# Optimization experiments

Measured on AMD Instinct MI355X. Metric: run time of the kernel, lower is better.

The kernel has to match this reference:

```python
import jax, jax.numpy as jnp
from jax import lax
import numpy as np

B, V, T, K, HE, TH, E, L = 128, 30000, 50, 50, 256, 800, 300, 3
DELTA = 0.005


def setup_inputs() -> dict:
    key = jax.random.key(0)
    ks = jax.random.split(key, 24)
    rn = lambda k, s, sc=0.05: jax.random.normal(k, s, jnp.float32) * sc
    return dict(
        X=jax.random.uniform(ks[0], (B, V), jnp.float32),
        timestamp=jax.random.randint(ks[1], (B,), 0, T),
        X_mean=jax.random.uniform(ks[2], (T, V), jnp.float32),
        W_eta_map=rn(ks[3], (HE, V)), b_eta_map=rn(ks[4], (HE,)),
        lstm_Wih=rn(ks[5], (L, 4 * HE, HE)), lstm_Whh=rn(ks[6], (L, 4 * HE, HE)),
        lstm_bih=rn(ks[7], (L, 4 * HE)), lstm_bhh=rn(ks[8], (L, 4 * HE)),
        W_qeta_mu=rn(ks[9], (K, HE + K)), b_qeta_mu=rn(ks[10], (K,)),
        W_qeta_ls=rn(ks[11], (K, HE + K)), b_qeta_ls=rn(ks[12], (K,)),
        W1=rn(ks[13], (TH, V + K)), b1=rn(ks[14], (TH,)),
        W2=rn(ks[15], (TH, TH)), b2=rn(ks[16], (TH,)),
        W_qt_mu=rn(ks[17], (K, TH)), b_qt_mu=rn(ks[18], (K,)),
        W_qt_ls=rn(ks[19], (K, TH)), b_qt_ls=rn(ks[20], (K,)),
        mu_q_alpha=rn(ks[21], (K, T, E), 0.1),
        logsigma_q_alpha=rn(ks[22], (K, T, E), 0.1),
        emb=rn(ks[23], (V, E), 0.1),
    )


def _lstm(x, Wih, Whh, bih, bhh):
    # PyTorch-style multi-layer LSTM, batch=1 squeezed away; x: [T, HE]
    for l in range(Wih.shape[0]):
        Wi, Wh, bi, bh = Wih[l], Whh[l], bih[l], bhh[l]
        def step(carry, xt, Wi=Wi, Wh=Wh, bi=bi, bh=bh):
            h, c = carry
            g = Wi @ xt + Wh @ h + bi + bh
            i, f, gg, o = jnp.split(g, 4)  # torch gate order i,f,g,o
            c = jax.nn.sigmoid(f) * c + jax.nn.sigmoid(i) * jnp.tanh(gg)
            h = jax.nn.sigmoid(o) * jnp.tanh(c)
            return (h, c), h
        H = Wh.shape[1]
        _, x = lax.scan(step, (jnp.zeros(H, x.dtype), jnp.zeros(H, x.dtype)), x)
    return x


def reference(X, timestamp, X_mean, W_eta_map, b_eta_map, lstm_Wih, lstm_Whh,
              lstm_bih, lstm_bhh, W_qeta_mu, b_qeta_mu, W_qeta_ls, b_qeta_ls,
              W1, b1, W2, b2, W_qt_mu, b_qt_mu, W_qt_ls, b_qt_ls,
              mu_q_alpha, logsigma_q_alpha, emb):
    # eval-mode DETM forward (reparameterize returns mu when not training)
    nb = X / X.sum(1, keepdims=True)
    logd = jnp.log(jnp.float32(DELTA))
    Tn = X_mean.shape[0]
    first = jnp.arange(Tn) == 0

    # --- eta: LSTM over time then sequential Gaussian recurrence ---
    rnn_out = _lstm(X_mean @ W_eta_map.T + b_eta_map, lstm_Wih, lstm_Whh, lstm_bih, lstm_bhh)  # [T,HE]
    Kn = W_qeta_mu.shape[0]

    def eta_step(eta_prev, xs):
        out_t, f = xs
        h = jnp.concatenate([out_t, eta_prev])
        mu = W_qeta_mu @ h + b_qeta_mu
        ls = W_qeta_ls @ h + b_qeta_ls
        p_ls = jnp.where(f, 0.0, logd)  # prior: N(0,I) at t=0, N(eta_{t-1}, delta) after
        kl = 0.5 * jnp.sum((jnp.exp(ls) + (mu - eta_prev) ** 2) / (jnp.exp(p_ls) + 1e-6) - 1.0 + p_ls - ls)
        return mu, (mu, kl)  # eval: eta_t = mu_t

    _, (etas, kls_eta) = lax.scan(eta_step, jnp.zeros(Kn, X.dtype), (rnn_out, first))
    kl_eta = kls_eta.sum()

    # --- theta ---
    eta_td = etas[timestamp]  # [B,K]
    h = jnp.tanh(jnp.concatenate([nb, eta_td], axis=1) @ W1.T + b1)
    h = jnp.tanh(h @ W2.T + b2)
    mu_t = h @ W_qt_mu.T + b_qt_mu
    ls_t = h @ W_qt_ls.T + b_qt_ls
    theta = jax.nn.softmax(mu_t, axis=-1)  # eval: z = mu
    kl_theta = (0.5 * jnp.sum((jnp.exp(ls_t) + (mu_t - eta_td) ** 2) / (1.0 + 1e-6) - 1.0 - ls_t, axis=-1)).sum()

    # --- alpha (eval: alpha_t = mu_q_alpha[:,t,:]) ---
    alphas = jnp.transpose(mu_q_alpha, (1, 0, 2))      # [T,K,E]
    q_ls = jnp.transpose(logsigma_q_alpha, (1, 0, 2))
    p_mu = jnp.concatenate([jnp.zeros_like(alphas[:1]), alphas[:-1]], axis=0)
    p_ls = jnp.where(first[:, None, None], 0.0, logd)
    kl_alpha = (0.5 * jnp.sum((jnp.exp(q_ls) + (alphas - p_mu) ** 2) / (jnp.exp(p_ls) + 1e-6) - 1.0 + p_ls - q_ls, axis=-1)).sum()

    # --- beta, likelihood ---
    beta = jax.nn.softmax(jnp.einsum('tke,ve->tkv', alphas, emb), axis=-1)  # [T,K,V]
    px = jnp.einsum('bk,bkv->bv', theta, beta[timestamp])
    lnpx = jnp.log(px + 1e-6)
    nll = (-lnpx * X).sum(-1).mean()
    return theta, lnpx, beta, nll, kl_alpha, kl_eta, kl_theta
```

## Files before the change

kernel.cpp:

```cpp
#include <hip/hip_runtime.h>
#include <math.h>

#define B_  128
#define V_  30000
#define T_  50
#define K_  50
#define HE_ 256
#define TH_ 800
#define E_  300
#define L_  3

#define LOGD_ (-5.2983173665480363f)

#define TM 64
#define TN 64
#define TK 16

__global__ __launch_bounds__(256) void gemm_nt(
    const float* __restrict__ A, int lda, int M,
    const float* __restrict__ B, int ldb, int N,
    int K,
    float* __restrict__ C, int ldc,
    const float* __restrict__ bias, int mode, int kchunk)
{
    __shared__ float As[TK][TM + 4];
    __shared__ float Bs[TK][TN + 4];
    const int tid = threadIdx.x;
    const int bm = blockIdx.y * TM;
    const int bn = blockIdx.x * TN;
    const int tx = tid & 15;
    const int ty = tid >> 4;
    const int lr = tid >> 2;
    const int lc = (tid & 3) << 2;

    float acc[4][4];
#pragma unroll
    for (int i = 0; i < 4; ++i)
#pragma unroll
        for (int j = 0; j < 4; ++j) acc[i][j] = 0.f;

    const int kbeg = blockIdx.z * kchunk;
    const int kend = min(K, kbeg + kchunk);

    for (int k0 = kbeg; k0 < kend; k0 += TK) {
        {
            float v0 = 0.f, v1 = 0.f, v2 = 0.f, v3 = 0.f;
            int gr = bm + lr;
            if (gr < M) {
                const float* p = A + (size_t)gr * lda + k0 + lc;
                int rem = K - (k0 + lc);
                if (rem >= 4) {
                    float2 a0 = *(const float2*)p;
                    float2 a1 = *(const float2*)(p + 2);
                    v0 = a0.x; v1 = a0.y; v2 = a1.x; v3 = a1.y;
                } else {
                    if (rem > 0) v0 = p[0];
                    if (rem > 1) v1 = p[1];
                    if (rem > 2) v2 = p[2];
                }
            }
            As[lc + 0][lr] = v0; As[lc + 1][lr] = v1;
            As[lc + 2][lr] = v2; As[lc + 3][lr] = v3;
        }
        {
            float v0 = 0.f, v1 = 0.f, v2 = 0.f, v3 = 0.f;
            int gr = bn + lr;
            if (gr < N) {
                const float* p = B + (size_t)gr * ldb + k0 + lc;
                int rem = K - (k0 + lc);
                if (rem >= 4) {
                    float2 a0 = *(const float2*)p;
                    float2 a1 = *(const float2*)(p + 2);
                    v0 = a0.x; v1 = a0.y; v2 = a1.x; v3 = a1.y;
                } else {
                    if (rem > 0) v0 = p[0];
                    if (rem > 1) v1 = p[1];
                    if (rem > 2) v2 = p[2];
                }
            }
            Bs[lc + 0][lr] = v0; Bs[lc + 1][lr] = v1;
            Bs[lc + 2][lr] = v2; Bs[lc + 3][lr] = v3;
        }
        __syncthreads();
#pragma unroll
        for (int kk = 0; kk < TK; ++kk) {
            float a[4], b[4];
#pragma unroll
            for (int i = 0; i < 4; ++i) a[i] = As[kk][ty * 4 + i];
#pragma unroll
            for (int j = 0; j < 4; ++j) b[j] = Bs[kk][tx * 4 + j];
#pragma unroll
            for (int i = 0; i < 4; ++i)
#pragma unroll
                for (int j = 0; j < 4; ++j) acc[i][j] += a[i] * b[j];
        }
        __syncthreads();
    }

#pragma unroll
    for (int i = 0; i < 4; ++i) {
        int row = bm + ty * 4 + i;
        if (row >= M) continue;
#pragma unroll
        for (int j = 0; j < 4; ++j) {
            int col = bn + tx * 4 + j;
            if (col >= N) continue;
            float v = acc[i][j];
            if (mode == 3) {
                atomicAdd(&C[(size_t)row * ldc + col], v);
            } else {
                if (mode == 1) v = tanhf(v + bias[col]);
                else if (mode == 2) v = v + bias[col];
                C[(size_t)row * ldc + col] = v;
            }
        }
    }
}

__global__ __launch_bounds__(256) void bias_act(
    float* __restrict__ C, const float* __restrict__ bias,
    int total, int N, int mode)
{
    int idx = blockIdx.x * 256 + threadIdx.x;
    if (idx >= total) return;
    int j = idx % N;
    float v = C[idx] + bias[j];
    if (mode == 1) v = tanhf(v);
    C[idx] = v;
}

__global__ __launch_bounds__(256) void rowsum_inv(const float* __restrict__ X,
                                                  float* __restrict__ inv)
{
    int b = blockIdx.x;
    const float4* p = (const float4*)(X + (size_t)b * V_);
    float s = 0.f;
    for (int i = threadIdx.x; i < V_ / 4; i += 256) {
        float4 v = p[i];
        s += v.x + v.y + v.z + v.w;
    }
    for (int off = 32; off; off >>= 1) s += __shfl_down(s, off);
    __shared__ float red[4];
    int wid = threadIdx.x >> 6, lane = threadIdx.x & 63;
    if (lane == 0) red[wid] = s;
    __syncthreads();
    if (threadIdx.x == 0) inv[b] = 1.f / (red[0] + red[1] + red[2] + red[3]);
}

#define NLB 32

__global__ __launch_bounds__(256) void lstm_all(
    const float* __restrict__ rnn_in,
    const float* __restrict__ Wih,
    const float* __restrict__ Whh,
    const float* __restrict__ bih,
    const float* __restrict__ bhh,
    float* __restrict__ houtA,
    float* __restrict__ houtB,
    float* __restrict__ houtF,
    float* __restrict__ hping,
    int* __restrict__ barcnt)
{
    __shared__ float sx[8 * 36];
    __shared__ float sh[8 * 36];
    __shared__ float sg[32];
    const int tid = threadIdx.x;
    const int blk = blockIdx.x;
    const int row_local = tid >> 3;
    const int chunk = tid & 7;
    const int gate = row_local >> 3;
    const int jloc = row_local & 7;
    const int gr = gate * HE_ + blk * 8 + jloc;
    const int seg = tid >> 5, sidx = tid & 31;

    for (int l = 0; l < L_; ++l) {
        float4 wih[8], whh[8];
        const float4* pi = (const float4*)(Wih + ((size_t)l * 4 * HE_ + gr) * HE_ + chunk * 32);
        const float4* pw = (const float4*)(Whh + ((size_t)l * 4 * HE_ + gr) * HE_ + chunk * 32);
#pragma unroll
        for (int q = 0; q < 8; ++q) { wih[q] = pi[q]; whh[q] = pw[q]; }
        const float bias = bih[l * 4 * HE_ + gr] + bhh[l * 4 * HE_ + gr];
        const float* xs = (l == 0) ? rnn_in : ((l == 1) ? houtA : houtB);
        float* hd = (l == 0) ? houtA : ((l == 1) ? houtB : houtF);
        float cst = 0.f;

        for (int t = 0; t < T_; ++t) {
            const int wb = t & 1, rb = wb ^ 1;
            float xv = xs[t * HE_ + tid];
            float hv = (t > 0) ? hping[rb * HE_ + tid] : 0.f;
            sx[seg * 36 + sidx] = xv;
            sh[seg * 36 + sidx] = hv;
            __syncthreads();

            float acc = 0.f;
#pragma unroll
            for (int q = 0; q < 8; ++q) {
                float4 a = *(const float4*)&sx[chunk * 36 + q * 4];
                float4 b = *(const float4*)&sh[chunk * 36 + q * 4];
                float4 wa = wih[q], wc = whh[q];
                acc += wa.x * a.x + wa.y * a.y + wa.z * a.z + wa.w * a.w
                     + wc.x * b.x + wc.y * b.y + wc.z * b.z + wc.w * b.w;
            }
            acc += __shfl_xor(acc, 1);
            acc += __shfl_xor(acc, 2);
            acc += __shfl_xor(acc, 4);
            if (chunk == 0) sg[row_local] = acc + bias;
            __syncthreads();

            if (tid < 8) {
                float gi = sg[tid], gf = sg[8 + tid], gg = sg[16 + tid], go = sg[24 + tid];
                float si = 1.f / (1.f + expf(-gi));
                float sf = 1.f / (1.f + expf(-gf));
                float so = 1.f / (1.f + expf(-go));
                cst = sf * cst + si * tanhf(gg);
                float hn = so * tanhf(cst);
                int j = blk * 8 + tid;
                hping[wb * HE_ + j] = hn;
                hd[t * HE_ + j] = hn;
            }

            if (tid < 64) __threadfence();
            __syncthreads();
            if (tid == 0) {
                atomicAdd(barcnt, 1);
                const int tgt = (l * T_ + t + 1) * NLB;
                while (atomicAdd(barcnt, 0) < tgt) __builtin_amdgcn_s_sleep(2);
                __threadfence();
            }
            __syncthreads();
        }
    }
}

__global__ __launch_bounds__(64) void eta_scan(
    const float* __restrict__ rnn_out,
    const float* __restrict__ Wmu, const float* __restrict__ bmu,
    const float* __restrict__ Wls, const float* __restrict__ bls,
    float* __restrict__ etas,
    float* __restrict__ kl_eta_out)
{
    __shared__ float hbuf[HE_ + K_];
    const int lane = threadIdx.x;
    if (lane < K_) hbuf[HE_ + lane] = 0.f;
    float kl = 0.f;
    __syncthreads();
    for (int t = 0; t < T_; ++t) {
        for (int i = lane; i < HE_; i += 64) hbuf[i] = rnn_out[t * HE_ + i];
        __syncthreads();
        float mu = 0.f;
        if (lane < K_) {
            const float* wm = Wmu + lane * (HE_ + K_);
            const float* wl = Wls + lane * (HE_ + K_);
            float am = 0.f, al = 0.f;
            for (int i = 0; i < HE_ + K_; ++i) {
                float hv = hbuf[i];
                am += wm[i] * hv;
                al += wl[i] * hv;
            }
            mu = am + bmu[lane];
            float ls = al + bls[lane];
            float eprev = hbuf[HE_ + lane];
            float pls = (t == 0) ? 0.f : LOGD_;
            float d = mu - eprev;
            kl += 0.5f * ((expf(ls) + d * d) / (expf(pls) + 1e-6f) - 1.f + pls - ls);
            etas[t * K_ + lane] = mu;
        }
        __syncthreads();
        if (lane < K_) hbuf[HE_ + lane] = mu;
        __syncthreads();
    }
    for (int off = 32; off; off >>= 1) kl += __shfl_down(kl, off);
    if (lane == 0) *kl_eta_out = kl;
}

__global__ __launch_bounds__(256) void h1_epilogue(
    const float* __restrict__ C1, const float* __restrict__ inv,
    const float* __restrict__ etas, const int* __restrict__ ts,
    const float* __restrict__ W1, const float* __restrict__ b1,
    float* __restrict__ h1)
{
    int idx = blockIdx.x * 256 + threadIdx.x;
    if (idx >= B_ * TH_) return;
    int b = idx / TH_, j = idx % TH_;
    const float* e = etas + ts[b] * K_;
    const float* w = W1 + (size_t)j * (V_ + K_) + V_;
    float s = 0.f;
#pragma unroll
    for (int k = 0; k < K_; ++k) s += e[k] * w[k];
    h1[idx] = tanhf(C1[idx] * inv[b] + s + b1[j]);
}

__global__ __launch_bounds__(64) void theta_kernel(
    const float* __restrict__ mu_t, const float* __restrict__ ls_t,
    const float* __restrict__ etas, const int* __restrict__ ts,
    float* __restrict__ theta, float* __restrict__ kl_out)
{
    int b = blockIdx.x;
    int lane = threadIdx.x;
    bool ok = lane < K_;
    float m = ok ? mu_t[b * K_ + lane] : -3.4e38f;
    float mx = m;
    for (int off = 32; off; off >>= 1) mx = fmaxf(mx, __shfl_down(mx, off));
    mx = __shfl(mx, 0);
    float e = ok ? expf(m - mx) : 0.f;
    float s = e;
    for (int off = 32; off; off >>= 1) s += __shfl_down(s, off);
    s = __shfl(s, 0);
    if (ok) theta[b * K_ + lane] = e / s;
    float kl = 0.f;
    if (ok) {
        float ls = ls_t[b * K_ + lane];
        float d = m - etas[ts[b] * K_ + lane];
        kl = 0.5f * ((expf(ls) + d * d) / (1.f + 1e-6f) - 1.f - ls);
    }
    for (int off = 32; off; off >>= 1) kl += __shfl_down(kl, off);
    if (lane == 0) atomicAdd(kl_out, kl);
}

__global__ __launch_bounds__(256) void transpose_alphas(
    const float* __restrict__ mu, float* __restrict__ out)
{
    int idx = blockIdx.x * 256 + threadIdx.x;
    if (idx >= T_ * K_ * E_) return;
    int t = idx / (K_ * E_);
    int r = idx % (K_ * E_);
    int k = r / E_;
    int e = r % E_;
    out[idx] = mu[((size_t)k * T_ + t) * E_ + e];
}

__global__ __launch_bounds__(256) void softmax_rows(float* __restrict__ logits)
{
    int row = blockIdx.x;
    float4* p4 = (float4*)(logits + (size_t)row * V_);
    float m = -3.4e38f, s = 0.f;
    for (int i = threadIdx.x; i < V_ / 4; i += 256) {
        float4 v = p4[i];
        float vm = fmaxf(fmaxf(v.x, v.y), fmaxf(v.z, v.w));
        if (vm > m) { s *= expf(m - vm); m = vm; }
        s += expf(v.x - m) + expf(v.y - m) + expf(v.z - m) + expf(v.w - m);
    }
    for (int off = 32; off; off >>= 1) {
        float om = __shfl_down(m, off);
        float os = __shfl_down(s, off);
        float nm = fmaxf(m, om);
        s = s * expf(m - nm) + os * expf(om - nm);
        m = nm;
    }
    __shared__ float redm[4], reds[4];
    __shared__ float fm, fs;
    int wid = threadIdx.x >> 6, lane = threadIdx.x & 63;
    if (lane == 0) { redm[wid] = m; reds[wid] = s; }
    __syncthreads();
    if (threadIdx.x == 0) {
        float M = fmaxf(fmaxf(redm[0], redm[1]), fmaxf(redm[2], redm[3]));
        float S = reds[0] * expf(redm[0] - M) + reds[1] * expf(redm[1] - M) +
                  reds[2] * expf(redm[2] - M) + reds[3] * expf(redm[3] - M);
        fm = M; fs = 1.f / S;
    }
    __syncthreads();
    float M = fm, IS = fs;
    for (int i = threadIdx.x; i < V_ / 4; i += 256) {
        float4 v = p4[i];
        v.x = expf(v.x - M) * IS;
        v.y = expf(v.y - M) * IS;
        v.z = expf(v.z - M) * IS;
        v.w = expf(v.w - M) * IS;
        p4[i] = v;
    }
}

__global__ __launch_bounds__(256) void px_kernel(
    const float* __restrict__ beta, const float* __restrict__ theta,
    const int* __restrict__ ts, const float* __restrict__ X,
    float* __restrict__ lnpx, float* __restrict__ nll_acc)
{
    __shared__ float sb[K_][256];
    int t = blockIdx.y;
    int tid = threadIdx.x;
    int v = blockIdx.x * 256 + tid;
    bool vok = v < V_;
    bool any = false;
    for (int b = 0; b < B_; ++b) any |= (ts[b] == t);
    if (!any) return;
    for (int k = 0; k < K_; ++k)
        sb[k][tid] = vok ? beta[((size_t)t * K_ + k) * V_ + v] : 0.f;
    __syncthreads();
    float acc = 0.f;
    for (int b = 0; b < B_; ++b) {
        if (ts[b] != t) continue;
        const float* th = theta + b * K_;
        float px = 0.f;
#pragma unroll
        for (int k = 0; k < K_; ++k) px += th[k] * sb[k][tid];
        float l = logf(px + 1e-6f);
        if (vok) {
            lnpx[(size_t)b * V_ + v] = l;
            acc += l * X[(size_t)b * V_ + v];
        }
    }
    for (int off = 32; off; off >>= 1) acc += __shfl_down(acc, off);
    __shared__ float red[4];
    int wid = tid >> 6, lane = tid & 63;
    if (lane == 0) red[wid] = acc;
    __syncthreads();
    if (tid == 0) atomicAdd(nll_acc, red[0] + red[1] + red[2] + red[3]);
}

__global__ __launch_bounds__(256) void kl_alpha_kernel(
    const float* __restrict__ mu, const float* __restrict__ lsig,
    float* __restrict__ out)
{
    int idx = blockIdx.x * 256 + threadIdx.x;
    float term = 0.f;
    if (idx < K_ * T_ * E_) {
        int r = idx % (T_ * E_);
        int t = r / E_;
        float a = mu[idx];
        float q = lsig[idx];
        float pmu = (t > 0) ? mu[idx - E_] : 0.f;
        float pls = (t > 0) ? LOGD_ : 0.f;
        float d = a - pmu;
        term = 0.5f * ((expf(q) + d * d) / (expf(pls) + 1e-6f) - 1.f + pls - q);
    }
    for (int off = 32; off; off >>= 1) term += __shfl_down(term, off);
    __shared__ float red[4];
    int wid = threadIdx.x >> 6, lane = threadIdx.x & 63;
    if (lane == 0) red[wid] = term;
    __syncthreads();
    if (threadIdx.x == 0) atomicAdd(out, red[0] + red[1] + red[2] + red[3]);
}

__global__ void finalize_nll(const float* __restrict__ acc, float* __restrict__ out)
{
    *out = -acc[0] * (1.f / (float)B_);
}

extern "C" void kernel_launch(void* const* d_in, const int* in_sizes, int n_in,
                              void* d_out, int out_size, void* d_ws, size_t ws_size,
                              hipStream_t stream)
{
    const float* X          = (const float*)d_in[0];
    const int*   ts         = (const int*)d_in[1];
    const float* X_mean     = (const float*)d_in[2];
    const float* W_eta_map  = (const float*)d_in[3];
    const float* b_eta_map  = (const float*)d_in[4];
    const float* lstm_Wih   = (const float*)d_in[5];
    const float* lstm_Whh   = (const float*)d_in[6];
    const float* lstm_bih   = (const float*)d_in[7];
    const float* lstm_bhh   = (const float*)d_in[8];
    const float* W_qeta_mu  = (const float*)d_in[9];
    const float* b_qeta_mu  = (const float*)d_in[10];
    const float* W_qeta_ls  = (const float*)d_in[11];
    const float* b_qeta_ls  = (const float*)d_in[12];
    const float* W1         = (const float*)d_in[13];
    const float* b1         = (const float*)d_in[14];
    const float* W2         = (const float*)d_in[15];
    const float* b2         = (const float*)d_in[16];
    const float* W_qt_mu    = (const float*)d_in[17];
    const float* b_qt_mu    = (const float*)d_in[18];
    const float* W_qt_ls    = (const float*)d_in[19];
    const float* b_qt_ls    = (const float*)d_in[20];
    const float* mu_q_alpha = (const float*)d_in[21];
    const float* ls_q_alpha = (const float*)d_in[22];
    const float* emb        = (const float*)d_in[23];

    float* out     = (float*)d_out;
    float* o_theta = out;
    float* o_lnpx  = out + (size_t)B_ * K_;
    float* o_beta  = o_lnpx + (size_t)B_ * V_;
    float* o_scal  = o_beta + (size_t)T_ * K_ * V_;

    float* ws = (float*)d_ws;
    float* w_inv   = ws;
    float* w_rnn   = ws + 128;
    float* w_seq0  = ws + 12928;
    float* w_seq1  = ws + 25728;
    float* w_houtA = ws + 38528;
    float* w_houtB = ws + 51328;
    float* w_hping = ws + 64128;
    float* w_barc  = ws + 64640;
    float* w_etas  = ws + 89728;
    float* w_h1    = ws + 92228;
    float* w_h2    = ws + 194628;
    float* w_mu    = ws + 297028;
    float* w_ls    = ws + 303428;
    float* w_nll   = ws + 309828;
    float* w_alph  = ws + 309832;
    (void)w_seq1;

    hipMemsetAsync(o_scal, 0, 4 * sizeof(float), stream);
    hipMemsetAsync(w_h1, 0, (size_t)(102400 + 102400 + 6400 + 6400 + 1) * sizeof(float), stream);
    hipMemsetAsync(w_rnn, 0, (size_t)T_ * HE_ * sizeof(float), stream);
    hipMemsetAsync(w_barc, 0, sizeof(int), stream);

    rowsum_inv<<<B_, 256, 0, stream>>>(X, w_inv);

    gemm_nt<<<dim3(HE_ / TN, 1, 125), 256, 0, stream>>>(
        X_mean, V_, T_, W_eta_map, V_, HE_, V_, w_rnn, HE_, nullptr, 3, 240);
    bias_act<<<(T_ * HE_ + 255) / 256, 256, 0, stream>>>(
        w_rnn, b_eta_map, T_ * HE_, HE_, 2);

    lstm_all<<<NLB, 256, 0, stream>>>(
        w_rnn, lstm_Wih, lstm_Whh, lstm_bih, lstm_bhh,
        w_houtA, w_houtB, w_seq0, w_hping, (int*)w_barc);

    eta_scan<<<1, 64, 0, stream>>>(w_seq0, W_qeta_mu, b_qeta_mu,
                                   W_qeta_ls, b_qeta_ls, w_etas, o_scal + 2);

    gemm_nt<<<dim3((TH_ + TN - 1) / TN, (B_ + TM - 1) / TM, 75), 256, 0, stream>>>(
        X, V_, B_, W1, V_ + K_, TH_, V_, w_h1, TH_, nullptr, 3, 400);
    h1_epilogue<<<(B_ * TH_ + 255) / 256, 256, 0, stream>>>(
        w_h1, w_inv, w_etas, ts, W1, b1, w_h1);

    gemm_nt<<<dim3((TH_ + TN - 1) / TN, (B_ + TM - 1) / TM, 10), 256, 0, stream>>>(
        w_h1, TH_, B_, W2, TH_, TH_, TH_, w_h2, TH_, nullptr, 3, 80);
    bias_act<<<(B_ * TH_ + 255) / 256, 256, 0, stream>>>(
        w_h2, b2, B_ * TH_, TH_, 1);

    gemm_nt<<<dim3(1, (B_ + TM - 1) / TM, 25), 256, 0, stream>>>(
        w_h2, TH_, B_, W_qt_mu, TH_, K_, TH_, w_mu, K_, nullptr, 3, 32);
    gemm_nt<<<dim3(1, (B_ + TM - 1) / TM, 25), 256, 0, stream>>>(
        w_h2, TH_, B_, W_qt_ls, TH_, K_, TH_, w_ls, K_, nullptr, 3, 32);
    bias_act<<<(B_ * K_ + 255) / 256, 256, 0, stream>>>(
        w_mu, b_qt_mu, B_ * K_, K_, 2);
    bias_act<<<(B_ * K_ + 255) / 256, 256, 0, stream>>>(
        w_ls, b_qt_ls, B_ * K_, K_, 2);

    theta_kernel<<<B_, 64, 0, stream>>>(w_mu, w_ls, w_etas, ts, o_theta, o_scal + 3);

    transpose_alphas<<<(T_ * K_ * E_ + 255) / 256, 256, 0, stream>>>(mu_q_alpha, w_alph);
    gemm_nt<<<dim3((V_ + TN - 1) / TN, (T_ * K_ + TM - 1) / TM, 1), 256, 0, stream>>>(
        w_alph, E_, T_ * K_, emb, E_, V_, E_, o_beta, V_, nullptr, 0, E_);
    softmax_rows<<<T_ * K_, 256, 0, stream>>>(o_beta);

    px_kernel<<<dim3((V_ + 255) / 256, T_), 256, 0, stream>>>(
        o_beta, o_theta, ts, X, o_lnpx, w_nll);

    kl_alpha_kernel<<<(K_ * T_ * E_ + 255) / 256, 256, 0, stream>>>(
        mu_q_alpha, ls_q_alpha, o_scal + 1);

    finalize_nll<<<1, 1, 0, stream>>>(w_nll, o_scal);
}
```

Measured before the change: 2.756 ms.

## Compute beta logits with split-bf16 MFMA and fuse exp into GEMM epilogue

Replaces the FP32 SIMT GEMM for the alpha·emb logits with an MFMA bf16 GEMM that splits each operand into high and low bf16 parts (three products) to approximate FP32 accuracy. The exp and row-sum are fused into the GEMM epilogue via atomics, and a separate pass normalizes. This drops the max-subtraction and the two-pass softmax reads. The eta_scan is also widened to 256 threads with 4-way split dot products. Skipping the max shift risks overflow if logits are large, and split-bf16 is slightly less precise than FP32.

```diff
diff --git a/kernel.cpp b/kernel.cpp
--- a/kernel.cpp
+++ b/kernel.cpp
@@ -11,6 +11,9 @@
 #define L_  3
 
 #define LOGD_ (-5.2983173665480363f)
+
+typedef short bf16x8 __attribute__((ext_vector_type(8)));
+typedef float f32x4  __attribute__((ext_vector_type(4)));
 
 #define TM 64
 #define TN 64
@@ -232,7 +235,7 @@
     }
 }
 
-__global__ __launch_bounds__(64) void eta_scan(
+__global__ __launch_bounds__(256) void eta_scan(
     const float* __restrict__ rnn_out,
     const float* __restrict__ Wmu, const float* __restrict__ bmu,
     const float* __restrict__ Wls, const float* __restrict__ bls,
@@ -240,37 +243,49 @@
     float* __restrict__ kl_eta_out)
 {
     __shared__ float hbuf[HE_ + K_];
-    const int lane = threadIdx.x;
-    if (lane < K_) hbuf[HE_ + lane] = 0.f;
+    __shared__ float smu[K_];
+    __shared__ float red[256];
+    const int tid = threadIdx.x;
+    const int k = tid >> 2, c = tid & 3;
+    if (tid < K_) hbuf[HE_ + tid] = 0.f;
     float kl = 0.f;
     __syncthreads();
     for (int t = 0; t < T_; ++t) {
-        for (int i = lane; i < HE_; i += 64) hbuf[i] = rnn_out[t * HE_ + i];
+        if (tid < HE_) hbuf[tid] = rnn_out[t * HE_ + tid];
         __syncthreads();
-        float mu = 0.f;
-        if (lane < K_) {
-            const float* wm = Wmu + lane * (HE_ + K_);
-            const float* wl = Wls + lane * (HE_ + K_);
+        if (k < K_) {
+            const float* wm = Wmu + k * (HE_ + K_);
+            const float* wl = Wls + k * (HE_ + K_);
             float am = 0.f, al = 0.f;
-            for (int i = 0; i < HE_ + K_; ++i) {
+            for (int i = c; i < HE_ + K_; i += 4) {
                 float hv = hbuf[i];
                 am += wm[i] * hv;
                 al += wl[i] * hv;
             }
-            mu = am + bmu[lane];
-            float ls = al + bls[lane];
-            float eprev = hbuf[HE_ + lane];
-            float pls = (t == 0) ? 0.f : LOGD_;
-            float d = mu - eprev;
-            kl += 0.5f * ((expf(ls) + d * d) / (expf(pls) + 1e-6f) - 1.f + pls - ls);
-            etas[t * K_ + lane] = mu;
+            am += __shfl_xor(am, 1); am += __shfl_xor(am, 2);
+            al += __shfl_xor(al, 1); al += __shfl_xor(al, 2);
+            if (c == 0) {
+                float mu = am + bmu[k];
+                float ls = al + bls[k];
+                float eprev = hbuf[HE_ + k];
+                float pls = (t == 0) ? 0.f : LOGD_;
+                float d = mu - eprev;
+                kl += 0.5f * ((expf(ls) + d * d) / (expf(pls) + 1e-6f) - 1.f + pls - ls);
+                etas[t * K_ + k] = mu;
+                smu[k] = mu;
+            }
         }
         __syncthreads();
-        if (lane < K_) hbuf[HE_ + lane] = mu;
+        if (tid < K_) hbuf[HE_ + tid] = smu[tid];
         __syncthreads();
     }
-    for (int off = 32; off; off >>= 1) kl += __shfl_down(kl, off);
-    if (lane == 0) *kl_eta_out = kl;
+    red[tid] = kl;
+    __syncthreads();
+    if (tid == 0) {
+        float s = 0.f;
+        for (int i = 0; i < 256; ++i) s += red[i];
+        *kl_eta_out = s;
+    }
 }
 
 __global__ __launch_bounds__(256) void h1_epilogue(
@@ -317,57 +332,169 @@
     if (lane == 0) atomicAdd(kl_out, kl);
 }
 
-__global__ __launch_bounds__(256) void transpose_alphas(
-    const float* __restrict__ mu, float* __restrict__ out)
+#define KP_   320
+#define MPAD_ 2560
+#define NPAD_ 30080
+
+__global__ __launch_bounds__(256) void conv_alpha(
+    const float* __restrict__ mu, short* __restrict__ Ah, short* __restrict__ Al)
 {
     int idx = blockIdx.x * 256 + threadIdx.x;
-    if (idx >= T_ * K_ * E_) return;
-    int t = idx / (K_ * E_);
-    int r = idx % (K_ * E_);
-    int k = r / E_;
-    int e = r % E_;
-    out[idx] = mu[((size_t)k * T_ + t) * E_ + e];
-}
-
-__global__ __launch_bounds__(256) void softmax_rows(float* __restrict__ logits)
-{
-    int row = blockIdx.x;
-    float4* p4 = (float4*)(logits + (size_t)row * V_);
-    float m = -3.4e38f, s = 0.f;
-    for (int i = threadIdx.x; i < V_ / 4; i += 256) {
-        float4 v = p4[i];
-        float vm = fmaxf(fmaxf(v.x, v.y), fmaxf(v.z, v.w));
-        if (vm > m) { s *= expf(m - vm); m = vm; }
-        s += expf(v.x - m) + expf(v.y - m) + expf(v.z - m) + expf(v.w - m);
-    }
-    for (int off = 32; off; off >>= 1) {
-        float om = __shfl_down(m, off);
-        float os = __shfl_down(s, off);
-        float nm = fmaxf(m, om);
-        s = s * expf(m - nm) + os * expf(om - nm);
-        m = nm;
-    }
-    __shared__ float redm[4], reds[4];
-    __shared__ float fm, fs;
-    int wid = threadIdx.x >> 6, lane = threadIdx.x & 63;
-    if (lane == 0) { redm[wid] = m; reds[wid] = s; }
-    __syncthreads();
-    if (threadIdx.x == 0) {
-        float M = fmaxf(fmaxf(redm[0], redm[1]), fmaxf(redm[2], redm[3]));
-        float S = reds[0] * expf(redm[0] - M) + reds[1] * expf(redm[1] - M) +
-                  reds[2] * expf(redm[2] - M) + reds[3] * expf(redm[3] - M);
-        fm = M; fs = 1.f / S;
-    }
-    __syncthreads();
-    float M = fm, IS = fs;
-    for (int i = threadIdx.x; i < V_ / 4; i += 256) {
-        float4 v = p4[i];
-        v.x = expf(v.x - M) * IS;
-        v.y = expf(v.y - M) * IS;
-        v.z = expf(v.z - M) * IS;
-        v.w = expf(v.w - M) * IS;
-        p4[i] = v;
-    }
+    if (idx >= MPAD_ * KP_) return;
+    int row = idx / KP_, e = idx % KP_;
+    float v = 0.f;
+    if (row < T_ * K_ && e < E_) {
+        int t = row / K_, k = row % K_;
+        v = mu[((size_t)k * T_ + t) * E_ + e];
+    }
+    unsigned int u = __float_as_uint(v);
+    Ah[idx] = (short)(u >> 16);
+    float hf = __uint_as_float(u & 0xFFFF0000u);
+    Al[idx] = (short)(__float_as_uint(v - hf) >> 16);
+}
+
+__global__ __launch_bounds__(256) void gemm_beta(
+    const short* __restrict__ Ah, const short* __restrict__ Al,
+    const float* __restrict__ Bf,
+    float* __restrict__ Cexp,
+    float* __restrict__ bsum)
+{
+    __shared__ __align__(16) short lds[4 * 8192];
+    const int tid = threadIdx.x;
+    const int lane = tid & 63;
+    const int w = tid >> 6;
+    const int wr = w >> 1, wc = w & 1;
+    const int bm = blockIdx.y * 128;
+    const int bn = blockIdx.x * 128;
+    const int l15 = lane & 15, l4 = lane >> 4;
+
+    f32x4 acc[4][4];
+#pragma unroll
+    for (int mi = 0; mi < 4; ++mi)
+#pragma unroll
+        for (int ni = 0; ni < 4; ++ni) acc[mi][ni] = (f32x4){0.f, 0.f, 0.f, 0.f};
+
+    for (int k0 = 0; k0 < KP_; k0 += 64) {
+#pragma unroll
+        for (int q = 0; q < 8; ++q) {
+            int L = q * 256 + tid;
+            int tile = L >> 10;
+            int c = L & 1023;
+            int r = c >> 3;
+            int k8 = (c & 7) ^ (r & 7);
+            const short* src = (tile ? Al : Ah) + (size_t)(bm + r) * KP_ + k0 + k8 * 8;
+            *(uint4*)&lds[(size_t)(tile * 1024 + c) * 8] = *(const uint4*)src;
+        }
+#pragma unroll
+        for (int q = 0; q < 4; ++q) {
+            int L = q * 256 + tid;
+            int r = L >> 3;
+            int k8 = (L & 7) ^ (r & 7);
+            int rg = bn + r;
+            int kb = k0 + k8 * 8;
+            float vv[8];
+            if (rg < V_ && kb + 8 <= E_) {
+                float4 u0 = *(const float4*)(Bf + (size_t)rg * E_ + kb);
+                float4 u1 = *(const float4*)(Bf + (size_t)rg * E_ + kb + 4);
+                vv[0] = u0.x; vv[1] = u0.y; vv[2] = u0.z; vv[3] = u0.w;
+                vv[4] = u1.x; vv[5] = u1.y; vv[6] = u1.z; vv[7] = u1.w;
+            } else {
+#pragma unroll
+                for (int e = 0; e < 8; ++e) {
+                    int kk = kb + e;
+                    vv[e] = (rg < V_ && kk < E_) ? Bf[(size_t)rg * E_ + kk] : 0.f;
+                }
+            }
+            unsigned int hpk[4], lpk[4];
+#pragma unroll
+            for (int e = 0; e < 8; e += 2) {
+                unsigned int u0 = __float_as_uint(vv[e]);
+                unsigned int u1 = __float_as_uint(vv[e + 1]);
+                hpk[e >> 1] = (u0 >> 16) | (u1 & 0xFFFF0000u);
+                float d0 = vv[e]     - __uint_as_float(u0 & 0xFFFF0000u);
+                float d1 = vv[e + 1] - __uint_as_float(u1 & 0xFFFF0000u);
+                lpk[e >> 1] = (__float_as_uint(d0) >> 16) | (__float_as_uint(d1) & 0xFFFF0000u);
+            }
+            uint4 hv; hv.x = hpk[0]; hv.y = hpk[1]; hv.z = hpk[2]; hv.w = hpk[3];
+            uint4 lv; lv.x = lpk[0]; lv.y = lpk[1]; lv.z = lpk[2]; lv.w = lpk[3];
+            *(uint4*)&lds[(size_t)(2048 + L) * 8] = hv;
+            *(uint4*)&lds[(size_t)(3072 + L) * 8] = lv;
+        }
+        __syncthreads();
+
+#pragma unroll
+        for (int ks = 0; ks < 2; ++ks) {
+            bf16x8 fah[4], fal[4], fbh[4], fbl[4];
+#pragma unroll
+            for (int mi = 0; mi < 4; ++mi) {
+                int r = wr * 64 + mi * 16 + l15;
+                int s = r * 8 + ((ks * 4 + l4) ^ (r & 7));
+                fah[mi] = *(const bf16x8*)&lds[(size_t)s * 8];
+                fal[mi] = *(const bf16x8*)&lds[(size_t)(1024 + s) * 8];
+            }
+#pragma unroll
+            for (int ni = 0; ni < 4; ++ni) {
+                int r = wc * 64 + ni * 16 + l15;
+                int s = r * 8 + ((ks * 4 + l4) ^ (r & 7));
+                fbh[ni] = *(const bf16x8*)&lds[(size_t)(2048 + s) * 8];
+                fbl[ni] = *(const bf16x8*)&lds[(size_t)(3072 + s) * 8];
+            }
+#pragma unroll
+            for (int mi = 0; mi < 4; ++mi)
+#pragma unroll
+                for (int ni = 0; ni < 4; ++ni) {
+                    acc[mi][ni] = __builtin_amdgcn_mfma_f32_16x16x32_bf16(
+                        fah[mi], fbh[ni], acc[mi][ni], 0, 0, 0);
+                    acc[mi][ni] = __builtin_amdgcn_mfma_f32_16x16x32_bf16(
+                        fah[mi], fbl[ni], acc[mi][ni], 0, 0, 0);
+                    acc[mi][ni] = __builtin_amdgcn_mfma_f32_16x16x32_bf16(
+                        fal[mi], fbh[ni], acc[mi][ni], 0, 0, 0);
+                }
+        }
+        __syncthreads();
+    }
+
+#pragma unroll
+    for (int mi = 0; mi < 4; ++mi) {
+#pragma unroll
+        for (int reg = 0; reg < 4; ++reg) {
+            int grow = bm + wr * 64 + mi * 16 + (l4 << 2) + reg;
+            float rs = 0.f;
+            float ex[4];
+#pragma unroll
+            for (int ni = 0; ni < 4; ++ni) {
+                int gcol = bn + wc * 64 + ni * 16 + l15;
+                float e = (gcol < V_) ? __expf(acc[mi][ni][reg]) : 0.f;
+                ex[ni] = e;
+                rs += e;
+            }
+            if (grow < T_ * K_) {
+#pragma unroll
+                for (int ni = 0; ni < 4; ++ni) {
+                    int gcol = bn + wc * 64 + ni * 16 + l15;
+                    if (gcol < V_) Cexp[(size_t)grow * V_ + gcol] = ex[ni];
+                }
+            }
+            rs += __shfl_xor(rs, 1);
+            rs += __shfl_xor(rs, 2);
+            rs += __shfl_xor(rs, 4);
+            rs += __shfl_xor(rs, 8);
+            if (l15 == 0 && grow < T_ * K_) atomicAdd(&bsum[grow], rs);
+        }
+    }
+}
+
+__global__ __launch_bounds__(256) void beta_scale(
+    float* __restrict__ beta, const float* __restrict__ bsum)
+{
+    int row = blockIdx.y;
+    int c4 = blockIdx.x * 256 + threadIdx.x;
+    if (c4 >= V_ / 4) return;
+    float inv = 1.f / bsum[row];
+    float4* p = (float4*)(beta + (size_t)row * V_) + c4;
+    float4 v = *p;
+    v.x *= inv; v.y *= inv; v.z *= inv; v.w *= inv;
+    *p = v;
 }
 
 __global__ __launch_bounds__(256) void px_kernel(
@@ -475,7 +602,6 @@
     float* w_inv   = ws;
     float* w_rnn   = ws + 128;
     float* w_seq0  = ws + 12928;
-    float* w_seq1  = ws + 25728;
     float* w_houtA = ws + 38528;
     float* w_houtB = ws + 51328;
     float* w_hping = ws + 64128;
@@ -486,13 +612,15 @@
     float* w_mu    = ws + 297028;
     float* w_ls    = ws + 303428;
     float* w_nll   = ws + 309828;
-    float* w_alph  = ws + 309832;
-    (void)w_seq1;
+    float* w_bsum  = ws + 309832;
+    short* w_Ah    = (short*)(ws + 312344);
+    short* w_Al    = (short*)(ws + 721944);
 
     hipMemsetAsync(o_scal, 0, 4 * sizeof(float), stream);
     hipMemsetAsync(w_h1, 0, (size_t)(102400 + 102400 + 6400 + 6400 + 1) * sizeof(float), stream);
     hipMemsetAsync(w_rnn, 0, (size_t)T_ * HE_ * sizeof(float), stream);
     hipMemsetAsync(w_barc, 0, sizeof(int), stream);
+    hipMemsetAsync(w_bsum, 0, (size_t)T_ * K_ * sizeof(float), stream);
 
     rowsum_inv<<<B_, 256, 0, stream>>>(X, w_inv);
 
@@ -505,8 +633,8 @@
         w_rnn, lstm_Wih, lstm_Whh, lstm_bih, lstm_bhh,
         w_houtA, w_houtB, w_seq0, w_hping, (int*)w_barc);
 
-    eta_scan<<<1, 64, 0, stream>>>(w_seq0, W_qeta_mu, b_qeta_mu,
-                                   W_qeta_ls, b_qeta_ls, w_etas, o_scal + 2);
+    eta_scan<<<1, 256, 0, stream>>>(w_seq0, W_qeta_mu, b_qeta_mu,
+                                    W_qeta_ls, b_qeta_ls, w_etas, o_scal + 2);
 
     gemm_nt<<<dim3((TH_ + TN - 1) / TN, (B_ + TM - 1) / TM, 75), 256, 0, stream>>>(
         X, V_, B_, W1, V_ + K_, TH_, V_, w_h1, TH_, nullptr, 3, 400);
@@ -529,10 +657,10 @@
 
     theta_kernel<<<B_, 64, 0, stream>>>(w_mu, w_ls, w_etas, ts, o_theta, o_scal + 3);
 
-    transpose_alphas<<<(T_ * K_ * E_ + 255) / 256, 256, 0, stream>>>(mu_q_alpha, w_alph);
-    gemm_nt<<<dim3((V_ + TN - 1) / TN, (T_ * K_ + TM - 1) / TM, 1), 256, 0, stream>>>(
-        w_alph, E_, T_ * K_, emb, E_, V_, E_, o_beta, V_, nullptr, 0, E_);
-    softmax_rows<<<T_ * K_, 256, 0, stream>>>(o_beta);
+    conv_alpha<<<(MPAD_ * KP_ + 255) / 256, 256, 0, stream>>>(mu_q_alpha, w_Ah, w_Al);
+    gemm_beta<<<dim3(NPAD_ / 128, MPAD_ / 128), 256, 0, stream>>>(
+        w_Ah, w_Al, emb, o_beta, w_bsum);
+    beta_scale<<<dim3((V_ / 4 + 255) / 256, T_ * K_), 256, 0, stream>>>(o_beta, w_bsum);
 
     px_kernel<<<dim3((V_ + 255) / 256, T_), 256, 0, stream>>>(
         o_beta, o_theta, ts, X, o_lnpx, w_nll);
```

After: 2.766 ms. No clear change (+0.4%).
